# Performance work log

Hardware: AMD Instinct MI355X
Metric: run time of the kernel (lower is better)

The kernel has to match this reference:

```python
import jax, jax.numpy as jnp
import numpy as np

N, T, H, KQ, V = 8, 256, 8, 128, 32  # batch, seq (Tq=Tk=T), heads, kq_dim, value_dim(=latent_dim)
SCALE = 1.0 / np.sqrt(KQ)


def setup_inputs() -> dict:
    k = jax.random.split(jax.random.key(0), 10)
    w = 0.05
    return {
        "value": jax.random.normal(k[0], (N, T, V), dtype=jnp.float32),
        "key": jax.random.normal(k[1], (N, T, KQ), dtype=jnp.float32),
        "query": jax.random.normal(k[2], (N, T, KQ), dtype=jnp.float32),
        "mask": jax.random.randint(k[3], (N, T, V), 0, 2, dtype=jnp.int32),
        # attn_linear[0]: query proj, attn_linear[1]: key proj (torch Linear: y = x @ W.T + b)
        "Wq": jax.random.normal(k[4], (H * KQ, KQ), dtype=jnp.float32) * w,
        "bq": jax.random.normal(k[5], (H * KQ,), dtype=jnp.float32) * w,
        "Wk": jax.random.normal(k[6], (H * KQ, KQ), dtype=jnp.float32) * w,
        "bk": jax.random.normal(k[7], (H * KQ,), dtype=jnp.float32) * w,
        "Wo": jax.random.normal(k[8], (V, H * V), dtype=jnp.float32) * w,  # attn_out: Linear(ld*H, ld), ld == V
        "bo": jax.random.normal(k[9], (V,), dtype=jnp.float32) * w,
    }


def reference(value, key, query, mask, Wq, bq, Wk, bk, Wo, bo):
    n, t, vdim = value.shape
    nq, tq, _ = query.shape
    nk, tk, _ = key.shape
    h = Wq.shape[0] // query.shape[-1]
    kq = query.shape[-1]

    # per-head projections: (N, H, T, KQ)
    hq = (query @ Wq.T + bq).reshape(nq, tq, h, kq).transpose(0, 2, 1, 3)
    hk = (key @ Wk.T + bk).reshape(nk, tk, h, kq).transpose(0, 2, 1, 3)

    # scores: (N, H, Tq, Tk), then broadcast per value-dim -> (N, H, Tq, Tk, V)
    scores = jnp.einsum("nhqd,nhkd->nhqk", hq, hk) * jnp.asarray(SCALE, value.dtype)
    scores = jnp.broadcast_to(scores[..., None], (n, h, tq, tk, vdim))

    # mask (N, Tk, V): mask[i,t,d]==0 means value[i,t,d] unobserved
    m = mask[:, None, None, :, :]  # (N,1,1,Tk,V)
    scores = jnp.where(m == 0, jnp.asarray(-1e9, scores.dtype), scores)

    p_attn = jax.nn.softmax(scores, axis=-2)  # softmax over Tk, per value-dim

    # weighted sum over keys: (N, H, Tq, V) -> (N, Tq, H*V)
    out = jnp.einsum("nhqkv,nkv->nqhv", p_attn, value).reshape(n, tq, h * vdim)
    out_rep = out @ Wo.T + bo  # (N, Tq, ld)
    return out_rep, p_attn
```

## Files before the change

kernel.cpp:

```cpp
#include <hip/hip_runtime.h>

#define N_ 8
#define T_ 256
#define H_ 8
#define KQ_ 128
#define V_ 32

typedef float f32x4 __attribute__((ext_vector_type(4)));

__global__ __launch_bounds__(256) void proj_kernel(
    const float* __restrict__ query, const float* __restrict__ key,
    const float* __restrict__ Wq, const float* __restrict__ bq,
    const float* __restrict__ Wk, const float* __restrict__ bk,
    float* __restrict__ hqT, float* __restrict__ hkT)
{
  int b = blockIdx.x;
  int dh = b & 1;
  int h  = (b >> 1) & 7;
  int n  = (b >> 4) & 7;
  int proj = (b >> 7) & 1;
  const float* src  = proj ? key : query;
  const float* W    = proj ? Wk  : Wq;
  const float* bias = proj ? bk  : bq;
  float* dst        = proj ? hkT : hqT;
  int d0 = dh * 64;

  __shared__ float qs[256 * 36];
  __shared__ float ws[64 * 36];

  int tl   = threadIdx.x & 31;
  int dsub = threadIdx.x >> 5;
  const float* qsrc = src + (size_t)n * T_ * KQ_;
  const float* wsrc = W + (size_t)(h * KQ_ + d0) * KQ_;

  float acc[8][8];
#pragma unroll
  for (int it = 0; it < 8; ++it)
#pragma unroll
    for (int dd = 0; dd < 8; ++dd) acc[it][dd] = 0.f;

  for (int kc = 0; kc < 4; ++kc) {
    if (kc) __syncthreads();
    {
      int r = threadIdx.x >> 3, c4 = (threadIdx.x & 7) * 4;
#pragma unroll
      for (int rep = 0; rep < 8; ++rep) {
        int row = r + rep * 32;
        *(float4*)&qs[row * 36 + c4] =
            *(const float4*)&qsrc[(size_t)row * KQ_ + kc * 32 + c4];
      }
#pragma unroll
      for (int rep = 0; rep < 2; ++rep) {
        int row = r + rep * 32;
        *(float4*)&ws[row * 36 + c4] =
            *(const float4*)&wsrc[(size_t)row * KQ_ + kc * 32 + c4];
      }
    }
    __syncthreads();

#pragma unroll 2
    for (int j0 = 0; j0 < 32; j0 += 4) {
      float4 qv[8];
#pragma unroll
      for (int it = 0; it < 8; ++it)
        qv[it] = *(const float4*)&qs[(tl + 32 * it) * 36 + j0];
#pragma unroll
      for (int dd = 0; dd < 8; ++dd) {
        float4 w4 = *(const float4*)&ws[(dsub * 8 + dd) * 36 + j0];
#pragma unroll
        for (int it = 0; it < 8; ++it) {
          acc[it][dd] = fmaf(qv[it].x, w4.x, acc[it][dd]);
          acc[it][dd] = fmaf(qv[it].y, w4.y, acc[it][dd]);
          acc[it][dd] = fmaf(qv[it].z, w4.z, acc[it][dd]);
          acc[it][dd] = fmaf(qv[it].w, w4.w, acc[it][dd]);
        }
      }
    }
  }

#pragma unroll
  for (int dd = 0; dd < 8; ++dd) {
    int d = d0 + dsub * 8 + dd;
    float bb = bias[h * KQ_ + d];
    size_t base = (((size_t)n * H_ + h) * KQ_ + d) * T_;
#pragma unroll
    for (int it = 0; it < 8; ++it)
      dst[base + it * 32 + tl] = acc[it][dd] + bb;
  }
}

__global__ __launch_bounds__(128) void attn_kernel(
    const float* __restrict__ hqT, const float* __restrict__ hkT,
    const int* __restrict__ mask, const float* __restrict__ value,
    float* __restrict__ p_out, float* __restrict__ out_ws)
{
  const float SCALE = 0.08838834764831845f;
  int b = blockIdx.x;
  int q0 = (b & 31) * 8;
  int h  = (b >> 5) & 7;
  int n  = b >> 8;
  int t  = threadIdx.x;
  int w  = t >> 6;
  int row0 = (n * H_ + h) * T_ + q0;

  __shared__ float hq_s[KQ_ * 12];
  __shared__ float e_s[T_ * 8];
  __shared__ float inv_s[8 * 32];
  __shared__ float wred[2 * 8];
  __shared__ float red_s[8 * 32];
  __shared__ float red_o[8 * 32];

  const float* hqbase = hqT + ((size_t)n * H_ + h) * KQ_ * T_;
  const float* hkbase = hkT + ((size_t)n * H_ + h) * KQ_ * T_;

#pragma unroll
  for (int rep = 0; rep < 8; ++rep) {
    int i = t + 128 * rep;
    int j = i >> 3, qq = i & 7;
    hq_s[j * 12 + qq] = hqbase[(size_t)j * T_ + q0 + qq];
  }
  __syncthreads();

  float acc[2][8];
#pragma unroll
  for (int i = 0; i < 2; ++i)
#pragma unroll
    for (int qq = 0; qq < 8; ++qq) acc[i][qq] = 0.f;

#pragma unroll 4
  for (int j = 0; j < KQ_; ++j) {
    float hk0 = hkbase[(size_t)j * T_ + t];
    float hk1 = hkbase[(size_t)j * T_ + t + 128];
    float4 a0 = *(const float4*)&hq_s[j * 12];
    float4 a1 = *(const float4*)&hq_s[j * 12 + 4];
    acc[0][0] = fmaf(a0.x, hk0, acc[0][0]); acc[0][1] = fmaf(a0.y, hk0, acc[0][1]);
    acc[0][2] = fmaf(a0.z, hk0, acc[0][2]); acc[0][3] = fmaf(a0.w, hk0, acc[0][3]);
    acc[0][4] = fmaf(a1.x, hk0, acc[0][4]); acc[0][5] = fmaf(a1.y, hk0, acc[0][5]);
    acc[0][6] = fmaf(a1.z, hk0, acc[0][6]); acc[0][7] = fmaf(a1.w, hk0, acc[0][7]);
    acc[1][0] = fmaf(a0.x, hk1, acc[1][0]); acc[1][1] = fmaf(a0.y, hk1, acc[1][1]);
    acc[1][2] = fmaf(a0.z, hk1, acc[1][2]); acc[1][3] = fmaf(a0.w, hk1, acc[1][3]);
    acc[1][4] = fmaf(a1.x, hk1, acc[1][4]); acc[1][5] = fmaf(a1.y, hk1, acc[1][5]);
    acc[1][6] = fmaf(a1.z, hk1, acc[1][6]); acc[1][7] = fmaf(a1.w, hk1, acc[1][7]);
  }

  float mloc[8];
#pragma unroll
  for (int qq = 0; qq < 8; ++qq) {
    float m = fmaxf(acc[0][qq], acc[1][qq]) * SCALE;
    for (int off = 32; off >= 1; off >>= 1)
      m = fmaxf(m, __shfl_xor(m, off, 64));
    mloc[qq] = m;
  }
  if ((t & 63) == 0) {
#pragma unroll
    for (int qq = 0; qq < 8; ++qq) wred[w * 8 + qq] = mloc[qq];
  }
  __syncthreads();
  {
#pragma unroll
    for (int qq = 0; qq < 8; ++qq) {
      float mx = fmaxf(wred[qq], wred[8 + qq]);
      acc[0][qq] = __expf(acc[0][qq] * SCALE - mx);
      acc[1][qq] = __expf(acc[1][qq] * SCALE - mx);
    }
    *(f32x4*)&e_s[t * 8]           = f32x4{acc[0][0], acc[0][1], acc[0][2], acc[0][3]};
    *(f32x4*)&e_s[t * 8 + 4]       = f32x4{acc[0][4], acc[0][5], acc[0][6], acc[0][7]};
    *(f32x4*)&e_s[(t + 128) * 8]     = f32x4{acc[1][0], acc[1][1], acc[1][2], acc[1][3]};
    *(f32x4*)&e_s[(t + 128) * 8 + 4] = f32x4{acc[1][4], acc[1][5], acc[1][6], acc[1][7]};
  }
  __syncthreads();

  const int*   mrow = mask  + (size_t)n * T_ * V_;
  const float* vrow = value + (size_t)n * T_ * V_;
  int v = t & 31, kg = t >> 5;
  float s8[8], o8[8];
#pragma unroll
  for (int qq = 0; qq < 8; ++qq) { s8[qq] = 0.f; o8[qq] = 0.f; }
#pragma unroll 4
  for (int i = 0; i < 64; ++i) {
    int k = kg * 64 + i;
    float mf = (float)mrow[k * V_ + v];
    float vv = vrow[k * V_ + v];
    float4 e0 = *(const float4*)&e_s[k * 8];
    float4 e1 = *(const float4*)&e_s[k * 8 + 4];
    float p;
    p = e0.x * mf; s8[0] += p; o8[0] = fmaf(p, vv, o8[0]);
    p = e0.y * mf; s8[1] += p; o8[1] = fmaf(p, vv, o8[1]);
    p = e0.z * mf; s8[2] += p; o8[2] = fmaf(p, vv, o8[2]);
    p = e0.w * mf; s8[3] += p; o8[3] = fmaf(p, vv, o8[3]);
    p = e1.x * mf; s8[4] += p; o8[4] = fmaf(p, vv, o8[4]);
    p = e1.y * mf; s8[5] += p; o8[5] = fmaf(p, vv, o8[5]);
    p = e1.z * mf; s8[6] += p; o8[6] = fmaf(p, vv, o8[6]);
    p = e1.w * mf; s8[7] += p; o8[7] = fmaf(p, vv, o8[7]);
  }
#pragma unroll
  for (int qq = 0; qq < 8; ++qq) {
    s8[qq] += __shfl_xor(s8[qq], 32, 64);
    o8[qq] += __shfl_xor(o8[qq], 32, 64);
  }
  if (w == 1 && (t & 63) < 32) {
#pragma unroll
    for (int qq = 0; qq < 8; ++qq) {
      red_s[qq * 32 + v] = s8[qq];
      red_o[qq * 32 + v] = o8[qq];
    }
  }
  __syncthreads();
  if (w == 0 && (t & 63) < 32) {
#pragma unroll
    for (int qq = 0; qq < 8; ++qq) {
      float s = s8[qq] + red_s[qq * 32 + v];
      float o = o8[qq] + red_o[qq * 32 + v];
      float inv = 1.0f / s;
      inv_s[qq * 32 + v] = inv;
      out_ws[(((size_t)n * T_ + q0 + qq) * H_ + h) * V_ + v] = o * inv;
    }
  }
  __syncthreads();

  {
    int v0 = (t & 7) * 4;
    f32x4 iv[8];
#pragma unroll
    for (int qq = 0; qq < 8; ++qq)
      iv[qq] = *(const f32x4*)&inv_s[qq * 32 + v0];
    f32x4* pbase = (f32x4*)p_out + (size_t)row0 * 2048;

#pragma unroll 4
    for (int rep = 0; rep < 16; ++rep) {
      int e4 = rep * 128 + t;
      int k  = rep * 16 + (t >> 3);
      const int4 m4 = *(const int4*)&mrow[k * V_ + v0];
      float fx = (float)m4.x, fy = (float)m4.y, fz = (float)m4.z, fw = (float)m4.w;
      f32x4 e0 = *(const f32x4*)&e_s[k * 8];
      f32x4 e1 = *(const f32x4*)&e_s[k * 8 + 4];
      float e[8] = {e0.x, e0.y, e0.z, e0.w, e1.x, e1.y, e1.z, e1.w};
#pragma unroll
      for (int qq = 0; qq < 8; ++qq) {
        f32x4 pv;
        pv.x = e[qq] * fx * iv[qq].x;
        pv.y = e[qq] * fy * iv[qq].y;
        pv.z = e[qq] * fz * iv[qq].z;
        pv.w = e[qq] * fw * iv[qq].w;
        __builtin_nontemporal_store(pv, &pbase[(size_t)qq * 2048 + e4]);
      }
    }
  }
}

__global__ __launch_bounds__(256) void outproj_kernel(
    const float* __restrict__ out_ws, const float* __restrict__ Wo,
    const float* __restrict__ bo, float* __restrict__ out_rep)
{
  __shared__ float wot[256 * 33];
  __shared__ float rows_s[4 * 256];
  __shared__ float red[4 * 32];
  int r0 = blockIdx.x * 4;
  for (int i = threadIdx.x; i < 32 * 256; i += 256) {
    int o = i >> 8, c = i & 255;
    wot[c * 33 + o] = Wo[i];
  }
  for (int i = threadIdx.x; i < 4 * 256; i += 256)
    rows_s[i] = out_ws[(size_t)r0 * 256 + i];
  __syncthreads();
  int o  = threadIdx.x & 31;
  int rr = (threadIdx.x >> 5) & 3;
  int kh = threadIdx.x >> 7;
  int cb = kh * 128;
  float acc = 0.f;
#pragma unroll 4
  for (int c = 0; c < 128; ++c)
    acc = fmaf(rows_s[rr * 256 + cb + c], wot[(cb + c) * 33 + o], acc);
  if (kh == 1) red[rr * 32 + o] = acc;
  __syncthreads();
  if (kh == 0)
    out_rep[(size_t)(r0 + rr) * 32 + o] = acc + red[rr * 32 + o] + bo[o];
}

extern "C" void kernel_launch(void* const* d_in, const int* in_sizes, int n_in,
                              void* d_out, int out_size, void* d_ws, size_t ws_size,
                              hipStream_t stream) {
  const float* value = (const float*)d_in[0];
  const float* key   = (const float*)d_in[1];
  const float* query = (const float*)d_in[2];
  const int*   mask  = (const int*)d_in[3];
  const float* Wq = (const float*)d_in[4];
  const float* bq = (const float*)d_in[5];
  const float* Wk = (const float*)d_in[6];
  const float* bk = (const float*)d_in[7];
  const float* Wo = (const float*)d_in[8];
  const float* bo = (const float*)d_in[9];

  float* out_rep = (float*)d_out;
  float* p_out   = (float*)d_out + (size_t)N_ * T_ * V_;

  float* hqT    = (float*)d_ws;
  float* hkT    = hqT + (size_t)N_ * H_ * KQ_ * T_;
  float* out_ws = hkT + (size_t)N_ * H_ * KQ_ * T_;

  hipLaunchKernelGGL(proj_kernel, dim3(256), dim3(256), 0, stream,
                     query, key, Wq, bq, Wk, bk, hqT, hkT);
  hipLaunchKernelGGL(attn_kernel, dim3(2048), dim3(128), 0, stream,
                     hqT, hkT, mask, value, p_out, out_ws);
  hipLaunchKernelGGL(outproj_kernel, dim3(512), dim3(256), 0, stream,
                     out_ws, Wo, bo, out_rep);
}
```

Before: 158.6 us.

## Widen attention blocks to 256 threads with one key per thread and padded LDS

The attention kernel now runs 256 threads per block instead of 128. Each thread computes scores for a single key rather than two, and the value accumulation is split across 8 key groups that are reduced through LDS instead of a shuffle-plus-pair reduction. The exp buffer row stride is padded from 8 to 9 floats to reduce LDS bank conflicts. This trades more parallelism per block for a larger LDS footprint and a cross-group reduction. Because the padded stride is odd, the float4 LDS accesses become misaligned, which may be split or mishandled.

```diff
diff --git a/kernel.cpp b/kernel.cpp
--- a/kernel.cpp
+++ b/kernel.cpp
@@ -5,6 +5,8 @@
 #define H_ 8
 #define KQ_ 128
 #define V_ 32
+#define QT_ 8
+#define EPAD 9
 
 typedef float f32x4 __attribute__((ext_vector_type(4)));
 
@@ -89,84 +91,83 @@
   }
 }
 
-__global__ __launch_bounds__(128) void attn_kernel(
+__global__ __launch_bounds__(256) void attn_kernel(
     const float* __restrict__ hqT, const float* __restrict__ hkT,
     const int* __restrict__ mask, const float* __restrict__ value,
     float* __restrict__ p_out, float* __restrict__ out_ws)
 {
   const float SCALE = 0.08838834764831845f;
   int b = blockIdx.x;
-  int q0 = (b & 31) * 8;
+  int q0 = (b & 31) * QT_;
   int h  = (b >> 5) & 7;
   int n  = b >> 8;
   int t  = threadIdx.x;
-  int w  = t >> 6;
   int row0 = (n * H_ + h) * T_ + q0;
 
-  __shared__ float hq_s[KQ_ * 12];
-  __shared__ float e_s[T_ * 8];
+  __shared__ float hq_s[KQ_ * 8];
+  __shared__ float e_s[T_ * EPAD];
+  __shared__ float wred[4 * 8];
+  __shared__ float red_s[8 * 8 * 32];
+  __shared__ float red_o[8 * 8 * 32];
   __shared__ float inv_s[8 * 32];
-  __shared__ float wred[2 * 8];
-  __shared__ float red_s[8 * 32];
-  __shared__ float red_o[8 * 32];
 
   const float* hqbase = hqT + ((size_t)n * H_ + h) * KQ_ * T_;
   const float* hkbase = hkT + ((size_t)n * H_ + h) * KQ_ * T_;
 
-#pragma unroll
-  for (int rep = 0; rep < 8; ++rep) {
-    int i = t + 128 * rep;
-    int j = i >> 3, qq = i & 7;
-    hq_s[j * 12 + qq] = hqbase[(size_t)j * T_ + q0 + qq];
-  }
-  __syncthreads();
-
-  float acc[2][8];
-#pragma unroll
-  for (int i = 0; i < 2; ++i)
-#pragma unroll
-    for (int qq = 0; qq < 8; ++qq) acc[i][qq] = 0.f;
-
+  {
+    int qq = t & 7, j0 = t >> 3;
+#pragma unroll
+    for (int rep = 0; rep < 4; ++rep) {
+      int j = j0 + rep * 32;
+      hq_s[j * 8 + qq] = hqbase[(size_t)j * T_ + q0 + qq];
+    }
+  }
+  __syncthreads();
+
+  float acc[8];
+#pragma unroll
+  for (int qq = 0; qq < 8; ++qq) acc[qq] = 0.f;
 #pragma unroll 4
   for (int j = 0; j < KQ_; ++j) {
-    float hk0 = hkbase[(size_t)j * T_ + t];
-    float hk1 = hkbase[(size_t)j * T_ + t + 128];
-    float4 a0 = *(const float4*)&hq_s[j * 12];
-    float4 a1 = *(const float4*)&hq_s[j * 12 + 4];
-    acc[0][0] = fmaf(a0.x, hk0, acc[0][0]); acc[0][1] = fmaf(a0.y, hk0, acc[0][1]);
-    acc[0][2] = fmaf(a0.z, hk0, acc[0][2]); acc[0][3] = fmaf(a0.w, hk0, acc[0][3]);
-    acc[0][4] = fmaf(a1.x, hk0, acc[0][4]); acc[0][5] = fmaf(a1.y, hk0, acc[0][5]);
-    acc[0][6] = fmaf(a1.z, hk0, acc[0][6]); acc[0][7] = fmaf(a1.w, hk0, acc[0][7]);
-    acc[1][0] = fmaf(a0.x, hk1, acc[1][0]); acc[1][1] = fmaf(a0.y, hk1, acc[1][1]);
-    acc[1][2] = fmaf(a0.z, hk1, acc[1][2]); acc[1][3] = fmaf(a0.w, hk1, acc[1][3]);
-    acc[1][4] = fmaf(a1.x, hk1, acc[1][4]); acc[1][5] = fmaf(a1.y, hk1, acc[1][5]);
-    acc[1][6] = fmaf(a1.z, hk1, acc[1][6]); acc[1][7] = fmaf(a1.w, hk1, acc[1][7]);
-  }
+    float hk = hkbase[(size_t)j * T_ + t];
+    float4 a0 = *(const float4*)&hq_s[j * 8];
+    float4 a1 = *(const float4*)&hq_s[j * 8 + 4];
+    acc[0] = fmaf(a0.x, hk, acc[0]);
+    acc[1] = fmaf(a0.y, hk, acc[1]);
+    acc[2] = fmaf(a0.z, hk, acc[2]);
+    acc[3] = fmaf(a0.w, hk, acc[3]);
+    acc[4] = fmaf(a1.x, hk, acc[4]);
+    acc[5] = fmaf(a1.y, hk, acc[5]);
+    acc[6] = fmaf(a1.z, hk, acc[6]);
+    acc[7] = fmaf(a1.w, hk, acc[7]);
+  }
+#pragma unroll
+  for (int qq = 0; qq < 8; ++qq) acc[qq] *= SCALE;
 
   float mloc[8];
 #pragma unroll
   for (int qq = 0; qq < 8; ++qq) {
-    float m = fmaxf(acc[0][qq], acc[1][qq]) * SCALE;
+    float m = acc[qq];
     for (int off = 32; off >= 1; off >>= 1)
       m = fmaxf(m, __shfl_xor(m, off, 64));
     mloc[qq] = m;
   }
   if ((t & 63) == 0) {
+    int w = t >> 6;
 #pragma unroll
     for (int qq = 0; qq < 8; ++qq) wred[w * 8 + qq] = mloc[qq];
   }
   __syncthreads();
   {
+    float ev[8];
 #pragma unroll
     for (int qq = 0; qq < 8; ++qq) {
-      float mx = fmaxf(wred[qq], wred[8 + qq]);
-      acc[0][qq] = __expf(acc[0][qq] * SCALE - mx);
-      acc[1][qq] = __expf(acc[1][qq] * SCALE - mx);
-    }
-    *(f32x4*)&e_s[t * 8]           = f32x4{acc[0][0], acc[0][1], acc[0][2], acc[0][3]};
-    *(f32x4*)&e_s[t * 8 + 4]       = f32x4{acc[0][4], acc[0][5], acc[0][6], acc[0][7]};
-    *(f32x4*)&e_s[(t + 128) * 8]     = f32x4{acc[1][0], acc[1][1], acc[1][2], acc[1][3]};
-    *(f32x4*)&e_s[(t + 128) * 8 + 4] = f32x4{acc[1][4], acc[1][5], acc[1][6], acc[1][7]};
+      float mx = fmaxf(fmaxf(wred[0*8+qq], wred[1*8+qq]),
+                       fmaxf(wred[2*8+qq], wred[3*8+qq]));
+      ev[qq] = __expf(acc[qq] - mx);
+    }
+    *(float4*)&e_s[t * EPAD]     = make_float4(ev[0], ev[1], ev[2], ev[3]);
+    *(float4*)&e_s[t * EPAD + 4] = make_float4(ev[4], ev[5], ev[6], ev[7]);
   }
   __syncthreads();
 
@@ -176,13 +177,12 @@
   float s8[8], o8[8];
 #pragma unroll
   for (int qq = 0; qq < 8; ++qq) { s8[qq] = 0.f; o8[qq] = 0.f; }
-#pragma unroll 4
-  for (int i = 0; i < 64; ++i) {
-    int k = kg * 64 + i;
+  for (int i = 0; i < 32; ++i) {
+    int k = kg * 32 + i;
     float mf = (float)mrow[k * V_ + v];
     float vv = vrow[k * V_ + v];
-    float4 e0 = *(const float4*)&e_s[k * 8];
-    float4 e1 = *(const float4*)&e_s[k * 8 + 4];
+    float4 e0 = *(const float4*)&e_s[k * EPAD];
+    float4 e1 = *(const float4*)&e_s[k * EPAD + 4];
     float p;
     p = e0.x * mf; s8[0] += p; o8[0] = fmaf(p, vv, o8[0]);
     p = e0.y * mf; s8[1] += p; o8[1] = fmaf(p, vv, o8[1]);
@@ -195,26 +195,21 @@
   }
 #pragma unroll
   for (int qq = 0; qq < 8; ++qq) {
-    s8[qq] += __shfl_xor(s8[qq], 32, 64);
-    o8[qq] += __shfl_xor(o8[qq], 32, 64);
-  }
-  if (w == 1 && (t & 63) < 32) {
-#pragma unroll
-    for (int qq = 0; qq < 8; ++qq) {
-      red_s[qq * 32 + v] = s8[qq];
-      red_o[qq * 32 + v] = o8[qq];
-    }
-  }
-  __syncthreads();
-  if (w == 0 && (t & 63) < 32) {
-#pragma unroll
-    for (int qq = 0; qq < 8; ++qq) {
-      float s = s8[qq] + red_s[qq * 32 + v];
-      float o = o8[qq] + red_o[qq * 32 + v];
-      float inv = 1.0f / s;
-      inv_s[qq * 32 + v] = inv;
-      out_ws[(((size_t)n * T_ + q0 + qq) * H_ + h) * V_ + v] = o * inv;
-    }
+    red_s[(kg * 8 + qq) * 32 + v] = s8[qq];
+    red_o[(kg * 8 + qq) * 32 + v] = o8[qq];
+  }
+  __syncthreads();
+  {
+    int qq = t >> 5, v2 = t & 31;
+    float s = 0.f, o = 0.f;
+#pragma unroll
+    for (int kg2 = 0; kg2 < 8; ++kg2) {
+      s += red_s[(kg2 * 8 + qq) * 32 + v2];
+      o += red_o[(kg2 * 8 + qq) * 32 + v2];
+    }
+    float inv = 1.0f / s;
+    inv_s[qq * 32 + v2] = inv;
+    out_ws[(((size_t)n * T_ + q0 + qq) * H_ + h) * V_ + v2] = o * inv;
   }
   __syncthreads();
 
@@ -226,14 +221,14 @@
       iv[qq] = *(const f32x4*)&inv_s[qq * 32 + v0];
     f32x4* pbase = (f32x4*)p_out + (size_t)row0 * 2048;
 
-#pragma unroll 4
-    for (int rep = 0; rep < 16; ++rep) {
-      int e4 = rep * 128 + t;
-      int k  = rep * 16 + (t >> 3);
+#pragma unroll
+    for (int rep = 0; rep < 8; ++rep) {
+      int e4 = rep * 256 + t;
+      int k  = rep * 32 + (t >> 3);
       const int4 m4 = *(const int4*)&mrow[k * V_ + v0];
       float fx = (float)m4.x, fy = (float)m4.y, fz = (float)m4.z, fw = (float)m4.w;
-      f32x4 e0 = *(const f32x4*)&e_s[k * 8];
-      f32x4 e1 = *(const f32x4*)&e_s[k * 8 + 4];
+      f32x4 e0 = *(const f32x4*)&e_s[k * EPAD];
+      f32x4 e1 = *(const f32x4*)&e_s[k * EPAD + 4];
       float e[8] = {e0.x, e0.y, e0.z, e0.w, e1.x, e1.y, e1.z, e1.w};
 #pragma unroll
       for (int qq = 0; qq < 8; ++qq) {
@@ -300,7 +295,7 @@
 
   hipLaunchKernelGGL(proj_kernel, dim3(256), dim3(256), 0, stream,
                      query, key, Wq, bq, Wk, bk, hqT, hkT);
-  hipLaunchKernelGGL(attn_kernel, dim3(2048), dim3(128), 0, stream,
+  hipLaunchKernelGGL(attn_kernel, dim3(2048), dim3(256), 0, stream,
                      hqT, hkT, mask, value, p_out, out_ws);
   hipLaunchKernelGGL(outproj_kernel, dim3(512), dim3(256), 0, stream,
                      out_ws, Wo, bo, out_rep);
```

After: 148.5 us, median of 2. -6.3%, faster.
